# Performance work log

Measured on AMD Instinct MI355X. Metric: run time of the kernel, lower is better.

## Reference

```python
import jax, jax.numpy as jnp
import numpy as np

B, L, D = 4, 2048, 1024
H, DH = 16, 64  # heads, head dim (D = H*DH)


def setup_inputs() -> dict:
    key = jax.random.key(0)
    k1, k2, k3 = jax.random.split(key, 3)
    scale = D ** -0.5
    xin = jax.random.normal(k1, (B, L, D), dtype=jnp.float32)
    W_qkv = jax.random.normal(k2, (D, 3 * D), dtype=jnp.float32) * scale
    W_o = jax.random.normal(k3, (D, D), dtype=jnp.float32) * scale
    return {"xin": xin, "W_qkv": W_qkv, "W_o": W_o}


def reference(xin, W_qkv, W_o):
    b, Lq, _ = xin.shape
    # QKV projection: (b, L, 3D). NOTE: original torch code reshapes the
    # (b, L, 3D) buffer directly to (b, 3, H, L, DH) — a non-standard axis
    # interleave — which we replicate faithfully.
    QKV = (xin @ W_qkv).reshape(b, 3, H, Lq, DH)
    Q, K, V = QKV[:, 0], QKV[:, 1], QKV[:, 2]  # each (b, H, L, DH)
    scores = jnp.einsum("bhqd,bhkd->bhqk", Q, K) * (DH ** -0.5)
    attn = jax.nn.softmax(scores, axis=-1)  # dropout_prob=0.0 -> identity
    out = jnp.einsum("bhqk,bhkd->bhqd", attn, V)
    out = out.transpose(0, 2, 1, 3).reshape(b, Lq, H * DH)
    return out @ W_o
```

## Files before the change

kernel.cpp:

```cpp
#include <hip/hip_runtime.h>
#include <stdint.h>

typedef short short8 __attribute__((ext_vector_type(8)));
typedef short short4v __attribute__((ext_vector_type(4)));
typedef float f32x4 __attribute__((ext_vector_type(4)));

#define LOG2E 1.44269504088896f
#define AS1 __attribute__((address_space(1)))
#define AS3 __attribute__((address_space(3)))

__device__ __forceinline__ float fexp2(float x) {
#if __has_builtin(__builtin_amdgcn_exp2f)
    return __builtin_amdgcn_exp2f(x);
#else
    return exp2f(x);
#endif
}
__device__ __forceinline__ unsigned short f2bfbits(float f) {
    unsigned x = __builtin_bit_cast(unsigned, f);
    unsigned r = x + 0x7fffu + ((x >> 16) & 1u);
    return (unsigned short)(r >> 16);
}
__device__ __forceinline__ float bfbits2f(unsigned short b) {
    unsigned u = ((unsigned)b) << 16;
    return __builtin_bit_cast(float, u);
}
__device__ __forceinline__ void unpack8(uint4 u, float4& f0, float4& f1) {
    f0.x = bfbits2f((unsigned short)(u.x & 0xffffu)); f0.y = bfbits2f((unsigned short)(u.x >> 16));
    f0.z = bfbits2f((unsigned short)(u.y & 0xffffu)); f0.w = bfbits2f((unsigned short)(u.y >> 16));
    f1.x = bfbits2f((unsigned short)(u.z & 0xffffu)); f1.y = bfbits2f((unsigned short)(u.z >> 16));
    f1.z = bfbits2f((unsigned short)(u.w & 0xffffu)); f1.w = bfbits2f((unsigned short)(u.w >> 16));
}
__device__ __forceinline__ unsigned pack2(float a, float b) {
    return (unsigned)f2bfbits(a) | ((unsigned)f2bfbits(b) << 16);
}
__device__ __forceinline__ unsigned pack2t(float a, float b) {
    unsigned ba = __builtin_bit_cast(unsigned, a);
    unsigned bb = __builtin_bit_cast(unsigned, b);
    return (ba >> 16) | (bb & 0xffff0000u);
}
__device__ __forceinline__ f32x4 mfma16(short4v a, short4v b, f32x4 c) {
#if __has_builtin(__builtin_amdgcn_mfma_f32_16x16x16bf16_1k)
    return __builtin_amdgcn_mfma_f32_16x16x16bf16_1k(a, b, c, 0, 0, 0);
#else
    asm("v_mfma_f32_16x16x16_bf16 %0, %1, %2, %0" : "+v"(c) : "v"(a), "v"(b));
    return c;
#endif
}
__device__ __forceinline__ void glds16(const void* gp, void* lp) {
    __builtin_amdgcn_global_load_lds((const AS1 unsigned*)(uintptr_t)gp,
                                     (AS3 unsigned*)(unsigned)(uintptr_t)lp, 16, 0, 0);
}

__global__ __launch_bounds__(256) void xbf_k(const float* __restrict__ x,
                                             unsigned short* __restrict__ y) {
    int i = (blockIdx.x * 256 + threadIdx.x) * 4;
    float4 v = *(const float4*)(x + i);
    uint2 u;
    u.x = pack2(v.x, v.y);
    u.y = pack2(v.z, v.w);
    *(uint2*)(y + i) = u;
}

__global__ __launch_bounds__(256) void t32cvt_k(const float* __restrict__ src,
                                                unsigned short* __restrict__ dst,
                                                int R, int C) {
    __shared__ float tile[32][36];
    int t = threadIdx.x;
    int bx = blockIdx.x, by = blockIdx.y;
    int r = t >> 3, c0 = (t & 7) * 4;
    *(float4*)&tile[r][c0] = *(const float4*)(src + (size_t)(by * 32 + r) * C + bx * 32 + c0);
    __syncthreads();
    uint2 u;
    u.x = pack2(tile[c0 + 0][r], tile[c0 + 1][r]);
    u.y = pack2(tile[c0 + 2][r], tile[c0 + 3][r]);
    *(uint2*)(dst + (size_t)(bx * 32 + r) * R + by * 32 + c0) = u;
}

template <bool CF32>
__global__ __launch_bounds__(256) void gemm_k(const unsigned short* __restrict__ A,
                                              const unsigned short* __restrict__ Bt,
                                              void* __restrict__ Cv,
                                              int M, int N, int K) {
    __shared__ unsigned short sA[128 * 32];
    __shared__ unsigned short sB[128 * 32];
    int t = threadIdx.x;
    int wid = t >> 6, lane = t & 63;
    int wm = (wid >> 1) * 64, wn = (wid & 1) * 64;
    int lm = lane & 15, lq = lane >> 4;
    size_t m0 = (size_t)blockIdx.y * 128, n0 = (size_t)blockIdx.x * 128;
    int srow = t >> 2, scol = (t & 3) * 8;
    const unsigned short* ga0 = A + (m0 + srow) * K + scol;
    const unsigned short* ga1 = A + (m0 + 64 + srow) * K + scol;
    const unsigned short* gb0 = Bt + (n0 + srow) * K + scol;
    const unsigned short* gb1 = Bt + (n0 + 64 + srow) * K + scol;
    unsigned short* laA0 = &sA[wid * 512];
    unsigned short* laA1 = &sA[2048 + wid * 512];
    unsigned short* laB0 = &sB[wid * 512];
    unsigned short* laB1 = &sB[2048 + wid * 512];
    f32x4 acc[4][4] = {};
    for (int k0 = 0; k0 < K; k0 += 32) {
        __syncthreads();
        glds16(ga0 + k0, laA0);
        glds16(ga1 + k0, laA1);
        glds16(gb0 + k0, laB0);
        glds16(gb1 + k0, laB1);
        __syncthreads();
        short8 af[4], bfr[4];
        #pragma unroll
        for (int i = 0; i < 4; ++i) af[i] = *(const short8*)&sA[(wm + i * 16 + lm) * 32 + lq * 8];
        #pragma unroll
        for (int j = 0; j < 4; ++j) bfr[j] = *(const short8*)&sB[(wn + j * 16 + lm) * 32 + lq * 8];
        #pragma unroll
        for (int i = 0; i < 4; ++i)
            #pragma unroll
            for (int j = 0; j < 4; ++j)
                acc[i][j] = __builtin_amdgcn_mfma_f32_16x16x32_bf16(af[i], bfr[j], acc[i][j], 0, 0, 0);
    }
    #pragma unroll
    for (int i = 0; i < 4; ++i)
        #pragma unroll
        for (int j = 0; j < 4; ++j)
            #pragma unroll
            for (int r = 0; r < 4; ++r) {
                size_t row = m0 + wm + i * 16 + lq * 4 + r;
                size_t col = n0 + wn + j * 16 + lm;
                if (CF32) ((float*)Cv)[row * N + col] = acc[i][j][r];
                else ((unsigned short*)Cv)[row * N + col] = f2bfbits(acc[i][j][r]);
            }
}

__global__ __launch_bounds__(256) void vt_k(const unsigned short* __restrict__ qkv,
                                            unsigned short* __restrict__ vt) {
    __shared__ unsigned short tile[64 * 72];
    int kt = blockIdx.x, bh = blockIdx.y;
    int b = bh >> 4, h = bh & 15;
    const unsigned short* Vp = qkv + (size_t)b * 6291456 + 4194304 + (size_t)h * 131072;
    int t = threadIdx.x;
    int row = t >> 2, cc = (t & 3) * 16;
    const unsigned short* src = Vp + (size_t)(kt * 64 + row) * 64 + cc;
    *(uint4*)&tile[row * 72 + cc] = *(const uint4*)src;
    *(uint4*)&tile[row * 72 + cc + 8] = *(const uint4*)(src + 8);
    __syncthreads();
    unsigned v[8];
    #pragma unroll
    for (int j = 0; j < 8; ++j) {
        unsigned short a = tile[(cc + 2 * j) * 72 + row];
        unsigned short bsh = tile[(cc + 2 * j + 1) * 72 + row];
        v[j] = (unsigned)a | ((unsigned)bsh << 16);
    }
    unsigned short* dst = vt + ((size_t)bh * 64 + row) * 2048 + kt * 64 + cc;
    *(uint4*)dst = make_uint4(v[0], v[1], v[2], v[3]);
    *(uint4*)(dst + 8) = make_uint4(v[4], v[5], v[6], v[7]);
}

__global__ __launch_bounds__(256, 4) void attn_mfma(const unsigned short* __restrict__ qkv,
                                                    const unsigned short* __restrict__ vt,
                                                    unsigned short* __restrict__ aout) {
    __shared__ unsigned short Ks[64 * 72];
    __shared__ unsigned short Vs[64 * 72];
    int bid = blockIdx.x;
    int qt = bid & 15, h = (bid >> 4) & 15, b = bid >> 8;
    int t = threadIdx.x;
    int wave = t >> 6, lane = t & 63, lm = lane & 15, quad = lane >> 4;
    const unsigned short* Qb = qkv + (size_t)b * 6291456 + (size_t)h * 131072;
    const unsigned short* Kb = Qb + 2097152;
    const unsigned short* Vtb = vt + (size_t)(b * 16 + h) * 131072;
    int q0 = qt * 128 + wave * 32;

    const float qs = 0.125f * LOG2E;
    short8 qf[2][2];
    #pragma unroll
    for (int i = 0; i < 2; ++i)
        #pragma unroll
        for (int c = 0; c < 2; ++c) {
            uint4 u = *(const uint4*)(Qb + (size_t)(q0 + i * 16 + lm) * 64 + c * 32 + quad * 8);
            float4 f0, f1; unpack8(u, f0, f1);
            uint4 v;
            v.x = pack2(f0.x * qs, f0.y * qs);
            v.y = pack2(f0.z * qs, f0.w * qs);
            v.z = pack2(f1.x * qs, f1.y * qs);
            v.w = pack2(f1.z * qs, f1.w * qs);
            qf[i][c] = *(short8*)&v;
        }

    short4v ones4;
    #pragma unroll
    for (int z = 0; z < 4; ++z) ones4[z] = (short)0x3F80;

    f32x4 o[2][4] = {};
    f32x4 l_acc[2] = {};

    int srow = t >> 2, scol = (t & 3) * 16;

    uint4 k0r, k1r, v0r, v1r;
    {
        const unsigned short* kp = Kb + (size_t)srow * 64 + scol;
        k0r = *(const uint4*)kp;
        k1r = *(const uint4*)(kp + 8);
        const unsigned short* vp = Vtb + (size_t)srow * 2048 + scol;
        v0r = *(const uint4*)vp;
        v1r = *(const uint4*)(vp + 8);
    }

    #pragma unroll 1
    for (int kt = 0; kt < 32; ++kt) {
        __syncthreads();
        *(uint4*)&Ks[srow * 72 + scol] = k0r;
        *(uint4*)&Ks[srow * 72 + scol + 8] = k1r;
        *(uint4*)&Vs[srow * 72 + scol] = v0r;
        *(uint4*)&Vs[srow * 72 + scol + 8] = v1r;
        __syncthreads();

        if (kt < 31) {
            const unsigned short* kp = Kb + (size_t)((kt + 1) * 64 + srow) * 64 + scol;
            k0r = *(const uint4*)kp;
            k1r = *(const uint4*)(kp + 8);
            const unsigned short* vp = Vtb + (size_t)srow * 2048 + (kt + 1) * 64 + scol;
            v0r = *(const uint4*)vp;
            v1r = *(const uint4*)(vp + 8);
        }

        short4v pf[2][4];
        #pragma unroll
        for (int j = 0; j < 4; ++j) {
            short8 kf0 = *(const short8*)&Ks[(j * 16 + lm) * 72 + quad * 8];
            short8 kf1 = *(const short8*)&Ks[(j * 16 + lm) * 72 + 32 + quad * 8];
            #pragma unroll
            for (int i = 0; i < 2; ++i) {
                f32x4 sf = {0.f, 0.f, 0.f, 0.f};
                sf = __builtin_amdgcn_mfma_f32_16x16x32_bf16(kf0, qf[i][0], sf, 0, 0, 0);
                sf = __builtin_amdgcn_mfma_f32_16x16x32_bf16(kf1, qf[i][1], sf, 0, 0, 0);
                uint2 u;
                u.x = pack2t(fexp2(sf[0]), fexp2(sf[1]));
                u.y = pack2t(fexp2(sf[2]), fexp2(sf[3]));
                pf[i][j] = *(short4v*)&u;
            }
        }

        #pragma unroll
        for (int jd = 0; jd < 4; ++jd)
            #pragma unroll
            for (int j = 0; j < 4; ++j) {
                short4v vf = *(const short4v*)&Vs[(jd * 16 + lm) * 72 + j * 16 + quad * 4];
                o[0][jd] = mfma16(pf[0][j], vf, o[0][jd]);
                o[1][jd] = mfma16(pf[1][j], vf, o[1][jd]);
            }
        #pragma unroll
        for (int j = 0; j < 4; ++j) {
            l_acc[0] = mfma16(pf[0][j], ones4, l_acc[0]);
            l_acc[1] = mfma16(pf[1][j], ones4, l_acc[1]);
        }
    }
    #pragma unroll
    for (int i = 0; i < 2; ++i)
        #pragma unroll
        for (int r = 0; r < 4; ++r) {
            float inv = 1.f / l_acc[i][r];
            int q = q0 + i * 16 + quad * 4 + r;
            size_t rowbase = ((size_t)b * 2048 + q) * 1024 + h * 64;
            #pragma unroll
            for (int jd = 0; jd < 4; ++jd)
                aout[rowbase + jd * 16 + lm] = f2bfbits(o[i][jd][r] * inv);
        }
}

extern "C" void kernel_launch(void* const* d_in, const int* in_sizes, int n_in,
                              void* d_out, int out_size, void* d_ws, size_t ws_size,
                              hipStream_t stream) {
    const float* xin  = (const float*)d_in[0];
    const float* wqkv = (const float*)d_in[1];
    const float* wo   = (const float*)d_in[2];
    float* out = (float*)d_out;

    char* ws = (char*)d_ws;
    unsigned short* qkv   = (unsigned short*)(ws);
    unsigned short* attn  = (unsigned short*)(ws + 50331648);
    unsigned short* wqkvT = (unsigned short*)(ws + 67108864);
    unsigned short* woT   = (unsigned short*)(ws + 73400320);
    unsigned short* vt    = (unsigned short*)(ws + 75497472);
    unsigned short* xb    = (unsigned short*)(ws + 92274688);

    dim3 blk(256);
    xbf_k<<<dim3(8192), blk, 0, stream>>>(xin, xb);
    t32cvt_k<<<dim3(3072 / 32, 1024 / 32), blk, 0, stream>>>(wqkv, wqkvT, 1024, 3072);
    t32cvt_k<<<dim3(1024 / 32, 1024 / 32), blk, 0, stream>>>(wo, woT, 1024, 1024);
    gemm_k<false><<<dim3(3072 / 128, 8192 / 128), blk, 0, stream>>>(xb, wqkvT, qkv, 8192, 3072, 1024);
    vt_k<<<dim3(32, 64), blk, 0, stream>>>(qkv, vt);
    attn_mfma<<<dim3(1024), blk, 0, stream>>>(qkv, vt, attn);
    gemm_k<true><<<dim3(1024 / 128, 8192 / 128), blk, 0, stream>>>(attn, woT, out, 8192, 1024, 1024);
}
```

Baseline: 292.1 us.

## Double-buffer attention K/V LDS tiles and swizzle block order in GEMM and attention

The attention kernel now keeps two LDS buffers for K and V and writes the next tile after the current compute, so each iteration needs one barrier instead of two. It also raises wave priority around the MFMA section. Both the GEMM and the attention kernel remap block indices so that consecutive workgroups spread across XCDs, which is meant to improve cache locality. LDS use doubles to about 36KB per block, which may limit occupancy at 4 blocks per CU.

```diff
diff --git a/kernel.cpp b/kernel.cpp
--- a/kernel.cpp
+++ b/kernel.cpp
@@ -88,7 +88,11 @@
     int wid = t >> 6, lane = t & 63;
     int wm = (wid >> 1) * 64, wn = (wid & 1) * 64;
     int lm = lane & 15, lq = lane >> 4;
-    size_t m0 = (size_t)blockIdx.y * 128, n0 = (size_t)blockIdx.x * 128;
+    int nwg = gridDim.x * gridDim.y;
+    int orig = blockIdx.y * gridDim.x + blockIdx.x;
+    int swz = (orig & 7) * (nwg >> 3) + (orig >> 3);
+    int bxi = swz % gridDim.x, byi = swz / gridDim.x;
+    size_t m0 = (size_t)byi * 128, n0 = (size_t)bxi * 128;
     int srow = t >> 2, scol = (t & 3) * 8;
     const unsigned short* ga0 = A + (m0 + srow) * K + scol;
     const unsigned short* ga1 = A + (m0 + 64 + srow) * K + scol;
@@ -157,9 +161,10 @@
 __global__ __launch_bounds__(256, 4) void attn_mfma(const unsigned short* __restrict__ qkv,
                                                     const unsigned short* __restrict__ vt,
                                                     unsigned short* __restrict__ aout) {
-    __shared__ unsigned short Ks[64 * 72];
-    __shared__ unsigned short Vs[64 * 72];
-    int bid = blockIdx.x;
+    __shared__ unsigned short Ks[2][64 * 72];
+    __shared__ unsigned short Vs[2][64 * 72];
+    int bid0 = blockIdx.x;
+    int bid = (bid0 & 7) * 128 + (bid0 >> 3);
     int qt = bid & 15, h = (bid >> 4) & 15, b = bid >> 8;
     int t = threadIdx.x;
     int wave = t >> 6, lane = t & 63, lm = lane & 15, quad = lane >> 4;
@@ -201,15 +206,14 @@
         const unsigned short* vp = Vtb + (size_t)srow * 2048 + scol;
         v0r = *(const uint4*)vp;
         v1r = *(const uint4*)(vp + 8);
+        *(uint4*)&Ks[0][srow * 72 + scol] = k0r;
+        *(uint4*)&Ks[0][srow * 72 + scol + 8] = k1r;
+        *(uint4*)&Vs[0][srow * 72 + scol] = v0r;
+        *(uint4*)&Vs[0][srow * 72 + scol + 8] = v1r;
     }
 
     #pragma unroll 1
     for (int kt = 0; kt < 32; ++kt) {
-        __syncthreads();
-        *(uint4*)&Ks[srow * 72 + scol] = k0r;
-        *(uint4*)&Ks[srow * 72 + scol + 8] = k1r;
-        *(uint4*)&Vs[srow * 72 + scol] = v0r;
-        *(uint4*)&Vs[srow * 72 + scol + 8] = v1r;
         __syncthreads();
 
         if (kt < 31) {
@@ -221,11 +225,15 @@
             v1r = *(const uint4*)(vp + 8);
         }
 
+        const unsigned short* ks = Ks[kt & 1];
+        const unsigned short* vs = Vs[kt & 1];
+        __builtin_amdgcn_s_setprio(1);
+
         short4v pf[2][4];
         #pragma unroll
         for (int j = 0; j < 4; ++j) {
-            short8 kf0 = *(const short8*)&Ks[(j * 16 + lm) * 72 + quad * 8];
-            short8 kf1 = *(const short8*)&Ks[(j * 16 + lm) * 72 + 32 + quad * 8];
+            short8 kf0 = *(const short8*)&ks[(j * 16 + lm) * 72 + quad * 8];
+            short8 kf1 = *(const short8*)&ks[(j * 16 + lm) * 72 + 32 + quad * 8];
             #pragma unroll
             for (int i = 0; i < 2; ++i) {
                 f32x4 sf = {0.f, 0.f, 0.f, 0.f};
@@ -242,7 +250,7 @@
         for (int jd = 0; jd < 4; ++jd)
             #pragma unroll
             for (int j = 0; j < 4; ++j) {
-                short4v vf = *(const short4v*)&Vs[(jd * 16 + lm) * 72 + j * 16 + quad * 4];
+                short4v vf = *(const short4v*)&vs[(jd * 16 + lm) * 72 + j * 16 + quad * 4];
                 o[0][jd] = mfma16(pf[0][j], vf, o[0][jd]);
                 o[1][jd] = mfma16(pf[1][j], vf, o[1][jd]);
             }
@@ -250,6 +258,16 @@
         for (int j = 0; j < 4; ++j) {
             l_acc[0] = mfma16(pf[0][j], ones4, l_acc[0]);
             l_acc[1] = mfma16(pf[1][j], ones4, l_acc[1]);
+        }
+        __builtin_amdgcn_s_setprio(0);
+
+        if (kt < 31) {
+            unsigned short* kd = Ks[(kt + 1) & 1];
+            unsigned short* vd = Vs[(kt + 1) & 1];
+            *(uint4*)&kd[srow * 72 + scol] = k0r;
+            *(uint4*)&kd[srow * 72 + scol + 8] = k1r;
+            *(uint4*)&vd[srow * 72 + scol] = v0r;
+            *(uint4*)&vd[srow * 72 + scol + 8] = v1r;
         }
     }
     #pragma unroll
```

After: 290.1 us. No clear change (-0.7%).
